# Performance work log

Measured on AMD Instinct MI355X. Metric: run time of the kernel, lower is better.

The kernel has to match this reference:

```python
import jax, jax.numpy as jnp
import numpy as np

D_MODEL = 768
N_CH = 2
D_STATE = 16
RANK = 8
LORA_SCALE = 2.0  # alpha/rank = (rank*2.0)/rank
N_LOOPS = 4       # MAX_INFER_LOOPS
BATCH = 1
SEQ = 1024
EPS = 1e-6        # RMSNorm eps


def setup_inputs() -> dict:
    key = jax.random.key(0)
    ks = jax.random.split(key, 12)
    f32 = jnp.float32
    n = lambda k, shp, s: jax.random.normal(k, shp, dtype=f32) * s
    return {
        "x": jax.random.normal(ks[0], (BATCH, SEQ, D_MODEL), dtype=f32),
        "in_proj_base": n(ks[1], (N_CH * D_MODEL, D_MODEL), 0.02),
        "lora_A": n(ks[2], (RANK, D_MODEL), 0.05),
        "lora_B": n(ks[3], (N_CH * D_MODEL, RANK), 0.05),
        "A_theta": n(ks[4], (N_CH, D_MODEL, D_STATE), 0.1),
        "B_real": n(ks[5], (N_CH, D_MODEL, D_STATE), 0.1),
        "B_imag": n(ks[6], (N_CH, D_MODEL, D_STATE), 0.1),
        "C_real": n(ks[7], (N_CH, D_MODEL, D_STATE), 0.1),
        "C_imag": n(ks[8], (N_CH, D_MODEL, D_STATE), 0.1),
        "out_proj_w": n(ks[9], (D_MODEL, N_CH * D_MODEL), 0.02),
        "mixer_norm_w": jnp.ones((D_MODEL,), f32),
        "loop_norm_w": jnp.ones((D_MODEL,), f32),
        "step_emb": n(ks[10], (N_LOOPS, D_MODEL), 0.02),
    }


def _rmsnorm(v, w):
    return v * jax.lax.rsqrt(jnp.mean(v * v, axis=-1, keepdims=True) + EPS) * w


def reference(x, in_proj_base, lora_A, lora_B, A_theta, B_real, B_imag,
              C_real, C_imag, out_proj_w, mixer_norm_w, loop_norm_w, step_emb):
    Bsz, Lsz, d = x.shape
    # LoRA-merged in_proj weight: base + scale * (B @ A)  [loop-invariant]
    W_in = in_proj_base + LORA_SCALE * (lora_B @ lora_A)  # [2d, d]
    cos_t = jnp.cos(A_theta)[None, None]  # [1,1,ch,d,s]
    sin_t = jnp.sin(A_theta)[None, None]
    Br = B_real[None, None]; Bi = B_imag[None, None]
    Cr = C_real[None, None]; Ci = C_imag[None, None]
    real = jnp.zeros((Bsz, Lsz, N_CH, d, D_STATE), x.dtype)
    imag = jnp.zeros_like(real)
    for i in range(N_LOOPS):  # fixed outer reasoning loop
        h = x + step_emb[i]
        # Mamba3ReasoningBlock: in_proj -> complex rotation state update -> sum over d_state
        x_in = (h @ W_in.T).reshape(Bsz, Lsz, N_CH, d)[..., None]  # [B,L,ch,d,1]
        new_real = cos_t * real - sin_t * imag + Br * x_in
        new_imag = sin_t * real + cos_t * imag + Bi * x_in
        y = (Cr * new_real - Ci * new_imag).sum(-1).reshape(Bsz, Lsz, N_CH * d)
        out = _rmsnorm(y @ out_proj_w.T, mixer_norm_w)
        x = _rmsnorm(h + out, loop_norm_w)  # residual + loop_norm
        real, imag = new_real, new_imag
    return x
```

## Files before the change

### kernel.cpp

```cpp
#include <hip/hip_runtime.h>

#define D_MODEL   768
#define TWO_D     1536
#define SEQ       1024
#define N_LOOPS   4
#define RANK      8
#define D_STATE   16
#define EPS       1e-6f

typedef unsigned short u16;
typedef short s16x8 __attribute__((ext_vector_type(8)));
typedef unsigned short u16x4 __attribute__((ext_vector_type(4)));
typedef float f32x4 __attribute__((ext_vector_type(4)));

__device__ inline u16 f2bf(float f) {
    union { float f; unsigned u; } v; v.f = f;
    unsigned r = v.u + 0x7fffu + ((v.u >> 16) & 1u);
    return (u16)(r >> 16);
}
__device__ inline float bf2f(u16 b) {
    union { unsigned u; float f; } v; v.u = ((unsigned)b) << 16;
    return v.f;
}

__global__ __launch_bounds__(256) void prep_all(
    const float* __restrict__ base, const float* __restrict__ lA,
    const float* __restrict__ lB,   const float* __restrict__ wout,
    const float* __restrict__ x,    const float* __restrict__ emb0,
    const float* __restrict__ th,   const float* __restrict__ Br,
    const float* __restrict__ Bi,   const float* __restrict__ Cr,
    const float* __restrict__ Ci,
    u16* __restrict__ Wbf, u16* __restrict__ Woutbf, float* __restrict__ G,
    float* __restrict__ hf, u16* __restrict__ hb)
{
    const int b = blockIdx.x, t = threadIdx.x;
    if (b < 1152) {
        int i0 = (b * 256 + t) * 4;
        int r = i0 / D_MODEL, c = i0 % D_MODEL;
        float4 a = *reinterpret_cast<const float4*>(&base[i0]);
#pragma unroll
        for (int k = 0; k < RANK; ++k) {
            float bk = 2.0f * lB[r * RANK + k];
            const float4 av = *reinterpret_cast<const float4*>(&lA[k * D_MODEL + c]);
            a.x += bk * av.x; a.y += bk * av.y; a.z += bk * av.z; a.w += bk * av.w;
        }
        u16x4 o; o.x = f2bf(a.x); o.y = f2bf(a.y); o.z = f2bf(a.z); o.w = f2bf(a.w);
        *reinterpret_cast<u16x4*>(&Wbf[i0]) = o;
    } else if (b < 2304) {
        int i0 = ((b - 1152) * 256 + t) * 4;
        const float4 v = *reinterpret_cast<const float4*>(&wout[i0]);
        u16x4 o; o.x = f2bf(v.x); o.y = f2bf(v.y); o.z = f2bf(v.z); o.w = f2bf(v.w);
        *reinterpret_cast<u16x4*>(&Woutbf[i0]) = o;
    } else if (b < 3072) {
        int i0 = ((b - 2304) * 256 + t) * 4;
        int d = i0 % D_MODEL;
        const float4 v = *reinterpret_cast<const float4*>(&x[i0]);
        const float4 e = *reinterpret_cast<const float4*>(&emb0[d]);
        float4 h = make_float4(v.x + e.x, v.y + e.y, v.z + e.z, v.w + e.w);
        *reinterpret_cast<float4*>(&hf[i0]) = h;
        u16x4 o; o.x = f2bf(h.x); o.y = f2bf(h.y); o.z = f2bf(h.z); o.w = f2bf(h.w);
        *reinterpret_cast<u16x4*>(&hb[i0]) = o;
    } else {
        int cd = (b - 3072) * 256 + t;
        if (cd >= TWO_D) return;
        float g0 = 0.f, g1 = 0.f, g2 = 0.f, g3 = 0.f;
        for (int s = 0; s < D_STATE; ++s) {
            int idx = cd * D_STATE + s;
            float tt = th[idx];
            float br = Br[idx], bi = Bi[idx];
            float cr = Cr[idx], ci = Ci[idx];
#pragma unroll
            for (int k = 0; k < 4; ++k) {
                float ck = cosf(k * tt), sk = sinf(k * tt);
                float er = ck * br - sk * bi;
                float ei = sk * br + ck * bi;
                float g  = cr * er - ci * ei;
                if (k == 0) g0 += g; else if (k == 1) g1 += g;
                else if (k == 2) g2 += g; else g3 += g;
            }
        }
        G[0 * TWO_D + cd] = g0; G[1 * TWO_D + cd] = g1;
        G[2 * TWO_D + cd] = g2; G[3 * TWO_D + cd] = g3;
    }
}

template<int K, int SPLITK, bool OUT_BF16>
__global__ __launch_bounds__(256) void gemm_nt(
    const u16* __restrict__ A, const u16* __restrict__ B,
    void* __restrict__ Cv, const int N)
{
    __shared__ u16 Al[64][72];
    __shared__ u16 Bl[64][72];
    const int t  = threadIdx.x;
    const int bm = blockIdx.y, bn = blockIdx.x, kz = blockIdx.z;
    const int lane = t & 63, w = t >> 6;
    const int wr = w >> 1, wc = w & 1;
    const int lr = lane & 15, kg = lane >> 4;

    const int KS = K / SPLITK;
    const int kbase = kz * KS;

    const int r0 = t >> 3;
    const int q0 = t & 7;
    const u16* Ag0 = A + (size_t)(bm * 64 + r0)      * K + kbase + q0 * 8;
    const u16* Ag1 = A + (size_t)(bm * 64 + r0 + 32) * K + kbase + q0 * 8;
    const u16* Bg0 = B + (size_t)(bn * 64 + r0)      * K + kbase + q0 * 8;
    const u16* Bg1 = B + (size_t)(bn * 64 + r0 + 32) * K + kbase + q0 * 8;

    uint4 ra0 = *reinterpret_cast<const uint4*>(Ag0);
    uint4 ra1 = *reinterpret_cast<const uint4*>(Ag1);
    uint4 rb0 = *reinterpret_cast<const uint4*>(Bg0);
    uint4 rb1 = *reinterpret_cast<const uint4*>(Bg1);

    f32x4 acc[2][2] = {};
    const int NKT = KS / 64;
    for (int kt = 0; kt < NKT; ++kt) {
        *reinterpret_cast<uint4*>(&Al[r0][q0 * 8])      = ra0;
        *reinterpret_cast<uint4*>(&Al[r0 + 32][q0 * 8]) = ra1;
        *reinterpret_cast<uint4*>(&Bl[r0][q0 * 8])      = rb0;
        *reinterpret_cast<uint4*>(&Bl[r0 + 32][q0 * 8]) = rb1;
        __syncthreads();
        if (kt + 1 < NKT) {
            const int ko = (kt + 1) * 64;
            ra0 = *reinterpret_cast<const uint4*>(Ag0 + ko);
            ra1 = *reinterpret_cast<const uint4*>(Ag1 + ko);
            rb0 = *reinterpret_cast<const uint4*>(Bg0 + ko);
            rb1 = *reinterpret_cast<const uint4*>(Bg1 + ko);
        }
#pragma unroll
        for (int ks = 0; ks < 2; ++ks) {
            const int ko = ks * 32 + kg * 8;
            s16x8 a0 = *reinterpret_cast<const s16x8*>(&Al[wr * 32 + lr][ko]);
            s16x8 a1 = *reinterpret_cast<const s16x8*>(&Al[wr * 32 + 16 + lr][ko]);
            s16x8 b0 = *reinterpret_cast<const s16x8*>(&Bl[wc * 32 + lr][ko]);
            s16x8 b1 = *reinterpret_cast<const s16x8*>(&Bl[wc * 32 + 16 + lr][ko]);
            acc[0][0] = __builtin_amdgcn_mfma_f32_16x16x32_bf16(a0, b0, acc[0][0], 0, 0, 0);
            acc[0][1] = __builtin_amdgcn_mfma_f32_16x16x32_bf16(a0, b1, acc[0][1], 0, 0, 0);
            acc[1][0] = __builtin_amdgcn_mfma_f32_16x16x32_bf16(a1, b0, acc[1][0], 0, 0, 0);
            acc[1][1] = __builtin_amdgcn_mfma_f32_16x16x32_bf16(a1, b1, acc[1][1], 0, 0, 0);
        }
        __syncthreads();
    }
    const int crow0 = bm * 64 + wr * 32 + kg * 4;
    const int ccol0 = bn * 64 + wc * 32 + lr;
#pragma unroll
    for (int m = 0; m < 2; ++m)
#pragma unroll
        for (int n = 0; n < 2; ++n)
#pragma unroll
            for (int r = 0; r < 4; ++r) {
                const int row = crow0 + m * 16 + r;
                const int col = ccol0 + n * 16;
                const float v = acc[m][n][r];
                if (OUT_BF16) ((u16*)Cv)[(size_t)row * N + col] = f2bf(v);
                else ((float*)Cv)[(size_t)kz * SEQ * N + (size_t)row * N + col] = v;
            }
}

__global__ __launch_bounds__(256) void y_kernel(
    const u16* __restrict__ xin,
    const float* __restrict__ G,
    const int nacc, u16* __restrict__ y)
{
    int i4 = blockIdx.x * 256 + threadIdx.x;
    int base = i4 * 4;
    int cd = base % TWO_D;
    float s0 = 0.f, s1 = 0.f, s2 = 0.f, s3 = 0.f;
    for (int j = 0; j < nacc; ++j) {
        u16x4 v = *reinterpret_cast<const u16x4*>(&xin[(size_t)j * SEQ * TWO_D + base]);
        const float4 g = *reinterpret_cast<const float4*>(&G[(size_t)(nacc - 1 - j) * TWO_D + cd]);
        s0 += bf2f(v.x) * g.x; s1 += bf2f(v.y) * g.y;
        s2 += bf2f(v.z) * g.z; s3 += bf2f(v.w) * g.w;
    }
    u16x4 o; o.x = f2bf(s0); o.y = f2bf(s1); o.z = f2bf(s2); o.w = f2bf(s3);
    *reinterpret_cast<u16x4*>(&y[base]) = o;
}

__global__ __launch_bounds__(256) void norm_kernel(
    const float* __restrict__ op0, const float* __restrict__ op1,
    const float* __restrict__ hprev,
    const float* __restrict__ mw,  const float* __restrict__ lw,
    const float* __restrict__ embn,
    float* __restrict__ dstf, u16* __restrict__ dstb)
{
    const int r = blockIdx.x * 4 + (threadIdx.x >> 6);
    const int lane = threadIdx.x & 63;
    const size_t ro = (size_t)r * D_MODEL;
    float op[12], h[12];
    float ss = 0.f;
#pragma unroll
    for (int e = 0; e < 12; ++e) {
        int d = lane + e * 64;
        op[e] = op0[ro + d] + op1[ro + d];
        h[e]  = hprev[ro + d];
        ss += op[e] * op[e];
    }
#pragma unroll
    for (int off = 32; off > 0; off >>= 1) ss += __shfl_xor(ss, off, 64);
    const float rs1 = rsqrtf(ss * (1.0f / D_MODEL) + EPS);
    float tt[12];
    float ss2 = 0.f;
#pragma unroll
    for (int e = 0; e < 12; ++e) {
        int d = lane + e * 64;
        tt[e] = h[e] + op[e] * rs1 * mw[d];
        ss2 += tt[e] * tt[e];
    }
#pragma unroll
    for (int off = 32; off > 0; off >>= 1) ss2 += __shfl_xor(ss2, off, 64);
    const float rs2 = rsqrtf(ss2 * (1.0f / D_MODEL) + EPS);
#pragma unroll
    for (int e = 0; e < 12; ++e) {
        int d = lane + e * 64;
        float xo = tt[e] * rs2 * lw[d];
        if (embn != nullptr) {
            float hn = xo + embn[d];
            dstf[ro + d] = hn;
            dstb[ro + d] = f2bf(hn);
        } else {
            dstf[ro + d] = xo;
        }
    }
}

extern "C" void kernel_launch(void* const* d_in, const int* in_sizes, int n_in,
                              void* d_out, int out_size, void* d_ws, size_t ws_size,
                              hipStream_t stream) {
    const float* x            = (const float*)d_in[0];
    const float* in_proj_base = (const float*)d_in[1];
    const float* lora_A       = (const float*)d_in[2];
    const float* lora_B       = (const float*)d_in[3];
    const float* A_theta      = (const float*)d_in[4];
    const float* B_real       = (const float*)d_in[5];
    const float* B_imag       = (const float*)d_in[6];
    const float* C_real       = (const float*)d_in[7];
    const float* C_imag       = (const float*)d_in[8];
    const float* out_proj_w   = (const float*)d_in[9];
    const float* mixer_w      = (const float*)d_in[10];
    const float* loop_w       = (const float*)d_in[11];
    const float* step_emb     = (const float*)d_in[12];
    float* out = (float*)d_out;

    char* p = (char*)d_ws;
    u16*   Wbf    = (u16*)p;   p += (size_t)TWO_D * D_MODEL * 2;
    u16*   Woutbf = (u16*)p;   p += (size_t)D_MODEL * TWO_D * 2;
    float* G      = (float*)p; p += (size_t)4 * TWO_D * 4;
    u16*   xin    = (u16*)p;   p += (size_t)N_LOOPS * SEQ * TWO_D * 2;
    u16*   ybf    = (u16*)p;   p += (size_t)SEQ * TWO_D * 2;
    float* hAf    = (float*)p; p += (size_t)SEQ * D_MODEL * 4;
    float* hBf    = (float*)p; p += (size_t)SEQ * D_MODEL * 4;
    u16*   hbf    = (u16*)p;   p += (size_t)SEQ * D_MODEL * 2;
    float* outpre = (float*)p; p += (size_t)2 * SEQ * D_MODEL * 4;

    prep_all<<<3078, 256, 0, stream>>>(
        in_proj_base, lora_A, lora_B, out_proj_w, x, step_emb,
        A_theta, B_real, B_imag, C_real, C_imag,
        Wbf, Woutbf, G, hAf, hbf);

    float* hcur = hAf;
    float* hnxt = hBf;
    for (int i = 0; i < N_LOOPS; ++i) {
        const bool last = (i == N_LOOPS - 1);
        gemm_nt<D_MODEL, 1, true><<<dim3(TWO_D / 64, SEQ / 64), 256, 0, stream>>>(
            hbf, Wbf, (void*)(xin + (size_t)i * SEQ * TWO_D), TWO_D);
        y_kernel<<<(SEQ * TWO_D / 4) / 256, 256, 0, stream>>>(xin, G, i + 1, ybf);
        gemm_nt<TWO_D, 2, false><<<dim3(D_MODEL / 64, SEQ / 64, 2), 256, 0, stream>>>(
            ybf, Woutbf, (void*)outpre, D_MODEL);
        norm_kernel<<<SEQ / 4, 256, 0, stream>>>(
            outpre, outpre + (size_t)SEQ * D_MODEL, hcur, mixer_w, loop_w,
            last ? nullptr : (step_emb + (size_t)(i + 1) * D_MODEL),
            last ? out : hnxt,
            last ? nullptr : hbf);
        float* tmp = hcur; hcur = hnxt; hnxt = tmp;
    }
}
```

Before: 228.7 us.

## Fold SSM coefficients into stacked out-proj weights and retile GEMM with direct LDS loads

Precomputes G-scaled copies of the out-projection weight for every loop lag and stores all in_proj outputs side by side. The out-projection GEMM then contracts over the concatenated history, so the separate y_kernel pass and its ybf buffer go away. The GEMM is retiled to 128x64 blocks and loads global data straight into LDS via global_load_lds, dropping the register-staged prefetch. The trade-off is a larger out-projection contraction that grows with the loop index, an unpadded LDS layout that may cause bank conflicts, and no overlap of loads with compute.

```diff
diff --git a/kernel.cpp b/kernel.cpp
--- a/kernel.cpp
+++ b/kernel.cpp
@@ -7,12 +7,22 @@
 #define RANK      8
 #define D_STATE   16
 #define EPS       1e-6f
+#define XIN_LD    (N_LOOPS * TWO_D)
 
 typedef unsigned short u16;
 typedef short s16x8 __attribute__((ext_vector_type(8)));
 typedef unsigned short u16x4 __attribute__((ext_vector_type(4)));
 typedef float f32x4 __attribute__((ext_vector_type(4)));
 
+#if defined(__has_builtin)
+#  if __has_builtin(__builtin_amdgcn_global_load_lds)
+#    define HAS_GLL 1
+#  endif
+#endif
+#ifndef HAS_GLL
+#  define HAS_GLL 0
+#endif
+
 __device__ inline u16 f2bf(float f) {
     union { float f; unsigned u; } v; v.f = f;
     unsigned r = v.u + 0x7fffu + ((v.u >> 16) & 1u);
@@ -23,14 +33,50 @@
     return v.f;
 }
 
+__device__ inline void gll16(const u16* g, u16* l) {
+#if HAS_GLL
+    __builtin_amdgcn_global_load_lds(
+        (__attribute__((address_space(1))) void*)(g),
+        (__attribute__((address_space(3))) void*)(l), 16, 0, 0);
+#else
+    const int ln = threadIdx.x & 63;
+    *reinterpret_cast<uint4*>(l + ln * 8) = *reinterpret_cast<const uint4*>(g);
+#endif
+}
+
+__global__ __launch_bounds__(256) void prep_g(
+    const float* __restrict__ th, const float* __restrict__ Br,
+    const float* __restrict__ Bi, const float* __restrict__ Cr,
+    const float* __restrict__ Ci, float* __restrict__ G)
+{
+    int cd = blockIdx.x * 256 + threadIdx.x;
+    if (cd >= TWO_D) return;
+    float g0 = 0.f, g1 = 0.f, g2 = 0.f, g3 = 0.f;
+    for (int s = 0; s < D_STATE; ++s) {
+        int idx = cd * D_STATE + s;
+        float tt = th[idx];
+        float br = Br[idx], bi = Bi[idx];
+        float cr = Cr[idx], ci = Ci[idx];
+#pragma unroll
+        for (int k = 0; k < 4; ++k) {
+            float ck = cosf(k * tt), sk = sinf(k * tt);
+            float er = ck * br - sk * bi;
+            float ei = sk * br + ck * bi;
+            float g  = cr * er - ci * ei;
+            if (k == 0) g0 += g; else if (k == 1) g1 += g;
+            else if (k == 2) g2 += g; else g3 += g;
+        }
+    }
+    G[0 * TWO_D + cd] = g0; G[1 * TWO_D + cd] = g1;
+    G[2 * TWO_D + cd] = g2; G[3 * TWO_D + cd] = g3;
+}
+
 __global__ __launch_bounds__(256) void prep_all(
     const float* __restrict__ base, const float* __restrict__ lA,
     const float* __restrict__ lB,   const float* __restrict__ wout,
     const float* __restrict__ x,    const float* __restrict__ emb0,
-    const float* __restrict__ th,   const float* __restrict__ Br,
-    const float* __restrict__ Bi,   const float* __restrict__ Cr,
-    const float* __restrict__ Ci,
-    u16* __restrict__ Wbf, u16* __restrict__ Woutbf, float* __restrict__ G,
+    const float* __restrict__ G,
+    u16* __restrict__ Wbf, u16* __restrict__ Wst,
     float* __restrict__ hf, u16* __restrict__ hb)
 {
     const int b = blockIdx.x, t = threadIdx.x;
@@ -46,13 +92,20 @@
         }
         u16x4 o; o.x = f2bf(a.x); o.y = f2bf(a.y); o.z = f2bf(a.z); o.w = f2bf(a.w);
         *reinterpret_cast<u16x4*>(&Wbf[i0]) = o;
-    } else if (b < 2304) {
+    } else if (b < 5760) {
         int i0 = ((b - 1152) * 256 + t) * 4;
-        const float4 v = *reinterpret_cast<const float4*>(&wout[i0]);
-        u16x4 o; o.x = f2bf(v.x); o.y = f2bf(v.y); o.z = f2bf(v.z); o.w = f2bf(v.w);
-        *reinterpret_cast<u16x4*>(&Woutbf[i0]) = o;
-    } else if (b < 3072) {
-        int i0 = ((b - 2304) * 256 + t) * 4;
+        int n = i0 / (4 * TWO_D);
+        int rem = i0 - n * 4 * TWO_D;
+        int m = rem / TWO_D;
+        int c = rem - m * TWO_D;
+        const float4 w = *reinterpret_cast<const float4*>(&wout[(size_t)n * TWO_D + c]);
+        const float4 g = *reinterpret_cast<const float4*>(&G[(size_t)(3 - m) * TWO_D + c]);
+        u16x4 o;
+        o.x = f2bf(w.x * g.x); o.y = f2bf(w.y * g.y);
+        o.z = f2bf(w.z * g.z); o.w = f2bf(w.w * g.w);
+        *reinterpret_cast<u16x4*>(&Wst[i0]) = o;
+    } else {
+        int i0 = ((b - 5760) * 256 + t) * 4;
         int d = i0 % D_MODEL;
         const float4 v = *reinterpret_cast<const float4*>(&x[i0]);
         const float4 e = *reinterpret_cast<const float4*>(&emb0[d]);
@@ -60,120 +113,68 @@
         *reinterpret_cast<float4*>(&hf[i0]) = h;
         u16x4 o; o.x = f2bf(h.x); o.y = f2bf(h.y); o.z = f2bf(h.z); o.w = f2bf(h.w);
         *reinterpret_cast<u16x4*>(&hb[i0]) = o;
-    } else {
-        int cd = (b - 3072) * 256 + t;
-        if (cd >= TWO_D) return;
-        float g0 = 0.f, g1 = 0.f, g2 = 0.f, g3 = 0.f;
-        for (int s = 0; s < D_STATE; ++s) {
-            int idx = cd * D_STATE + s;
-            float tt = th[idx];
-            float br = Br[idx], bi = Bi[idx];
-            float cr = Cr[idx], ci = Ci[idx];
-#pragma unroll
-            for (int k = 0; k < 4; ++k) {
-                float ck = cosf(k * tt), sk = sinf(k * tt);
-                float er = ck * br - sk * bi;
-                float ei = sk * br + ck * bi;
-                float g  = cr * er - ci * ei;
-                if (k == 0) g0 += g; else if (k == 1) g1 += g;
-                else if (k == 2) g2 += g; else g3 += g;
-            }
-        }
-        G[0 * TWO_D + cd] = g0; G[1 * TWO_D + cd] = g1;
-        G[2 * TWO_D + cd] = g2; G[3 * TWO_D + cd] = g3;
-    }
-}
-
-template<int K, int SPLITK, bool OUT_BF16>
+    }
+}
+
+template<bool OUT_BF16>
 __global__ __launch_bounds__(256) void gemm_nt(
-    const u16* __restrict__ A, const u16* __restrict__ B,
-    void* __restrict__ Cv, const int N)
-{
-    __shared__ u16 Al[64][72];
-    __shared__ u16 Bl[64][72];
-    const int t  = threadIdx.x;
+    const u16* __restrict__ A, const int lda,
+    const u16* __restrict__ B, const int ldb,
+    const int Kz, void* __restrict__ Cv, const int ldc)
+{
+    __shared__ __align__(16) u16 Al[128 * 64];
+    __shared__ __align__(16) u16 Bl[64 * 64];
+    const int t = threadIdx.x;
     const int bm = blockIdx.y, bn = blockIdx.x, kz = blockIdx.z;
     const int lane = t & 63, w = t >> 6;
-    const int wr = w >> 1, wc = w & 1;
+    const int wm = w >> 1, wn = w & 1;
     const int lr = lane & 15, kg = lane >> 4;
-
-    const int KS = K / SPLITK;
-    const int kbase = kz * KS;
-
-    const int r0 = t >> 3;
-    const int q0 = t & 7;
-    const u16* Ag0 = A + (size_t)(bm * 64 + r0)      * K + kbase + q0 * 8;
-    const u16* Ag1 = A + (size_t)(bm * 64 + r0 + 32) * K + kbase + q0 * 8;
-    const u16* Bg0 = B + (size_t)(bn * 64 + r0)      * K + kbase + q0 * 8;
-    const u16* Bg1 = B + (size_t)(bn * 64 + r0 + 32) * K + kbase + q0 * 8;
-
-    uint4 ra0 = *reinterpret_cast<const uint4*>(Ag0);
-    uint4 ra1 = *reinterpret_cast<const uint4*>(Ag1);
-    uint4 rb0 = *reinterpret_cast<const uint4*>(Bg0);
-    uint4 rb1 = *reinterpret_cast<const uint4*>(Bg1);
-
-    f32x4 acc[2][2] = {};
-    const int NKT = KS / 64;
-    for (int kt = 0; kt < NKT; ++kt) {
-        *reinterpret_cast<uint4*>(&Al[r0][q0 * 8])      = ra0;
-        *reinterpret_cast<uint4*>(&Al[r0 + 32][q0 * 8]) = ra1;
-        *reinterpret_cast<uint4*>(&Bl[r0][q0 * 8])      = rb0;
-        *reinterpret_cast<uint4*>(&Bl[r0 + 32][q0 * 8]) = rb1;
+    const int kbase = kz * Kz;
+
+    const u16* Aga = A + (size_t)(bm * 128 + w * 32 + (lane >> 3)) * lda + kbase + (lane & 7) * 8;
+    const u16* Bga = B + (size_t)(bn * 64  + w * 16 + (lane >> 3)) * ldb + kbase + (lane & 7) * 8;
+    u16* Alp = &Al[(w * 32) * 64];
+    u16* Blp = &Bl[(w * 16) * 64];
+
+    f32x4 acc[4][2] = {};
+    for (int k0 = 0; k0 < Kz; k0 += 64) {
+#pragma unroll
+        for (int q = 0; q < 4; ++q) gll16(Aga + (size_t)q * 8 * lda + k0, Alp + q * 512);
+#pragma unroll
+        for (int q = 0; q < 2; ++q) gll16(Bga + (size_t)q * 8 * ldb + k0, Blp + q * 512);
         __syncthreads();
-        if (kt + 1 < NKT) {
-            const int ko = (kt + 1) * 64;
-            ra0 = *reinterpret_cast<const uint4*>(Ag0 + ko);
-            ra1 = *reinterpret_cast<const uint4*>(Ag1 + ko);
-            rb0 = *reinterpret_cast<const uint4*>(Bg0 + ko);
-            rb1 = *reinterpret_cast<const uint4*>(Bg1 + ko);
-        }
 #pragma unroll
         for (int ks = 0; ks < 2; ++ks) {
-            const int ko = ks * 32 + kg * 8;
-            s16x8 a0 = *reinterpret_cast<const s16x8*>(&Al[wr * 32 + lr][ko]);
-            s16x8 a1 = *reinterpret_cast<const s16x8*>(&Al[wr * 32 + 16 + lr][ko]);
-            s16x8 b0 = *reinterpret_cast<const s16x8*>(&Bl[wc * 32 + lr][ko]);
-            s16x8 b1 = *reinterpret_cast<const s16x8*>(&Bl[wc * 32 + 16 + lr][ko]);
-            acc[0][0] = __builtin_amdgcn_mfma_f32_16x16x32_bf16(a0, b0, acc[0][0], 0, 0, 0);
-            acc[0][1] = __builtin_amdgcn_mfma_f32_16x16x32_bf16(a0, b1, acc[0][1], 0, 0, 0);
-            acc[1][0] = __builtin_amdgcn_mfma_f32_16x16x32_bf16(a1, b0, acc[1][0], 0, 0, 0);
-            acc[1][1] = __builtin_amdgcn_mfma_f32_16x16x32_bf16(a1, b1, acc[1][1], 0, 0, 0);
+            const int co = ks * 32 + kg * 8;
+            s16x8 a[4], b[2];
+#pragma unroll
+            for (int m = 0; m < 4; ++m)
+                a[m] = *reinterpret_cast<const s16x8*>(&Al[(wm * 64 + m * 16 + lr) * 64 + co]);
+#pragma unroll
+            for (int n = 0; n < 2; ++n)
+                b[n] = *reinterpret_cast<const s16x8*>(&Bl[(wn * 32 + n * 16 + lr) * 64 + co]);
+#pragma unroll
+            for (int m = 0; m < 4; ++m)
+#pragma unroll
+                for (int n = 0; n < 2; ++n)
+                    acc[m][n] = __builtin_amdgcn_mfma_f32_16x16x32_bf16(a[m], b[n], acc[m][n], 0, 0, 0);
         }
         __syncthreads();
     }
-    const int crow0 = bm * 64 + wr * 32 + kg * 4;
-    const int ccol0 = bn * 64 + wc * 32 + lr;
-#pragma unroll
-    for (int m = 0; m < 2; ++m)
+    const int row0 = bm * 128 + wm * 64 + kg * 4;
+    const int col0 = bn * 64 + wn * 32 + lr;
+#pragma unroll
+    for (int m = 0; m < 4; ++m)
 #pragma unroll
         for (int n = 0; n < 2; ++n)
 #pragma unroll
             for (int r = 0; r < 4; ++r) {
-                const int row = crow0 + m * 16 + r;
-                const int col = ccol0 + n * 16;
+                const int row = row0 + m * 16 + r;
+                const int col = col0 + n * 16;
                 const float v = acc[m][n][r];
-                if (OUT_BF16) ((u16*)Cv)[(size_t)row * N + col] = f2bf(v);
-                else ((float*)Cv)[(size_t)kz * SEQ * N + (size_t)row * N + col] = v;
+                if (OUT_BF16) ((u16*)Cv)[(size_t)row * ldc + col] = f2bf(v);
+                else ((float*)Cv)[(size_t)kz * SEQ * ldc + (size_t)row * ldc + col] = v;
             }
-}
-
-__global__ __launch_bounds__(256) void y_kernel(
-    const u16* __restrict__ xin,
-    const float* __restrict__ G,
-    const int nacc, u16* __restrict__ y)
-{
-    int i4 = blockIdx.x * 256 + threadIdx.x;
-    int base = i4 * 4;
-    int cd = base % TWO_D;
-    float s0 = 0.f, s1 = 0.f, s2 = 0.f, s3 = 0.f;
-    for (int j = 0; j < nacc; ++j) {
-        u16x4 v = *reinterpret_cast<const u16x4*>(&xin[(size_t)j * SEQ * TWO_D + base]);
-        const float4 g = *reinterpret_cast<const float4*>(&G[(size_t)(nacc - 1 - j) * TWO_D + cd]);
-        s0 += bf2f(v.x) * g.x; s1 += bf2f(v.y) * g.y;
-        s2 += bf2f(v.z) * g.z; s3 += bf2f(v.w) * g.w;
-    }
-    u16x4 o; o.x = f2bf(s0); o.y = f2bf(s1); o.z = f2bf(s2); o.w = f2bf(s3);
-    *reinterpret_cast<u16x4*>(&y[base]) = o;
 }
 
 __global__ __launch_bounds__(256) void norm_kernel(
@@ -243,34 +244,30 @@
 
     char* p = (char*)d_ws;
     u16*   Wbf    = (u16*)p;   p += (size_t)TWO_D * D_MODEL * 2;
-    u16*   Woutbf = (u16*)p;   p += (size_t)D_MODEL * TWO_D * 2;
+    u16*   Wst    = (u16*)p;   p += (size_t)D_MODEL * 4 * TWO_D * 2;
     float* G      = (float*)p; p += (size_t)4 * TWO_D * 4;
-    u16*   xin    = (u16*)p;   p += (size_t)N_LOOPS * SEQ * TWO_D * 2;
-    u16*   ybf    = (u16*)p;   p += (size_t)SEQ * TWO_D * 2;
-    float* hAf    = (float*)p; p += (size_t)SEQ * D_MODEL * 4;
-    float* hBf    = (float*)p; p += (size_t)SEQ * D_MODEL * 4;
+    u16*   xin    = (u16*)p;   p += (size_t)SEQ * XIN_LD * 2;
+    float* hf     = (float*)p; p += (size_t)SEQ * D_MODEL * 4;
     u16*   hbf    = (u16*)p;   p += (size_t)SEQ * D_MODEL * 2;
     float* outpre = (float*)p; p += (size_t)2 * SEQ * D_MODEL * 4;
 
-    prep_all<<<3078, 256, 0, stream>>>(
-        in_proj_base, lora_A, lora_B, out_proj_w, x, step_emb,
-        A_theta, B_real, B_imag, C_real, C_imag,
-        Wbf, Woutbf, G, hAf, hbf);
-
-    float* hcur = hAf;
-    float* hnxt = hBf;
+    prep_g<<<6, 256, 0, stream>>>(A_theta, B_real, B_imag, C_real, C_imag, G);
+    prep_all<<<6528, 256, 0, stream>>>(
+        in_proj_base, lora_A, lora_B, out_proj_w, x, step_emb, G,
+        Wbf, Wst, hf, hbf);
+
     for (int i = 0; i < N_LOOPS; ++i) {
         const bool last = (i == N_LOOPS - 1);
-        gemm_nt<D_MODEL, 1, true><<<dim3(TWO_D / 64, SEQ / 64), 256, 0, stream>>>(
-            hbf, Wbf, (void*)(xin + (size_t)i * SEQ * TWO_D), TWO_D);
-        y_kernel<<<(SEQ * TWO_D / 4) / 256, 256, 0, stream>>>(xin, G, i + 1, ybf);
-        gemm_nt<TWO_D, 2, false><<<dim3(D_MODEL / 64, SEQ / 64, 2), 256, 0, stream>>>(
-            ybf, Woutbf, (void*)outpre, D_MODEL);
+        gemm_nt<true><<<dim3(TWO_D / 64, SEQ / 128, 1), 256, 0, stream>>>(
+            hbf, D_MODEL, Wbf, D_MODEL, D_MODEL,
+            (void*)(xin + (size_t)i * TWO_D), XIN_LD);
+        gemm_nt<false><<<dim3(D_MODEL / 64, SEQ / 128, 2), 256, 0, stream>>>(
+            xin, XIN_LD, Wst + (size_t)(3 - i) * TWO_D, XIN_LD,
+            (i + 1) * D_MODEL, (void*)outpre, D_MODEL);
         norm_kernel<<<SEQ / 4, 256, 0, stream>>>(
-            outpre, outpre + (size_t)SEQ * D_MODEL, hcur, mixer_w, loop_w,
+            outpre, outpre + (size_t)SEQ * D_MODEL, hf, mixer_w, loop_w,
             last ? nullptr : (step_emb + (size_t)(i + 1) * D_MODEL),
-            last ? out : hnxt,
+            last ? out : hf,
             last ? nullptr : hbf);
-        float* tmp = hcur; hcur = hnxt; hnxt = tmp;
-    }
-}
+    }
+}
```

Measured after the change: 319.4 us. +39.7%, slower.

## Use direct global-to-LDS loads, raise split-K, fuse partial reduction into y kernel

Applied to the files above, without the earlier changes.

The GEMM now loads tiles with global_load_lds straight into unpadded LDS instead of staging through registers, and drops the register prefetch. The in-proj GEMM becomes split-K by 2 writing fp32 partials that y_kernel sums, rounds to bf16 and stores into the xin history. The out-proj uses split-K by 4, and norm_kernel reduces four partials. This adds blocks to fill more CUs, at the cost of extra fp32 partial traffic, no load/compute overlap, and possible LDS bank conflicts from removing the padding. norm now writes h in place, which is safe since each row reads before it writes.

```diff
diff --git a/kernel.cpp b/kernel.cpp
--- a/kernel.cpp
+++ b/kernel.cpp
@@ -13,6 +13,15 @@
 typedef unsigned short u16x4 __attribute__((ext_vector_type(4)));
 typedef float f32x4 __attribute__((ext_vector_type(4)));
 
+#if defined(__has_builtin)
+#  if __has_builtin(__builtin_amdgcn_global_load_lds)
+#    define HAS_GLL 1
+#  endif
+#endif
+#ifndef HAS_GLL
+#  define HAS_GLL 0
+#endif
+
 __device__ inline u16 f2bf(float f) {
     union { float f; unsigned u; } v; v.f = f;
     unsigned r = v.u + 0x7fffu + ((v.u >> 16) & 1u);
@@ -21,6 +30,17 @@
 __device__ inline float bf2f(u16 b) {
     union { unsigned u; float f; } v; v.u = ((unsigned)b) << 16;
     return v.f;
+}
+
+__device__ inline void gll16(const u16* g, u16* l) {
+#if HAS_GLL
+    __builtin_amdgcn_global_load_lds(
+        (__attribute__((address_space(1))) void*)(g),
+        (__attribute__((address_space(3))) void*)(l), 16, 0, 0);
+#else
+    const int ln = threadIdx.x & 63;
+    *reinterpret_cast<uint4*>(l + ln * 8) = *reinterpret_cast<const uint4*>(g);
+#endif
 }
 
 __global__ __launch_bounds__(256) void prep_all(
@@ -84,56 +104,39 @@
     }
 }
 
-template<int K, int SPLITK, bool OUT_BF16>
 __global__ __launch_bounds__(256) void gemm_nt(
-    const u16* __restrict__ A, const u16* __restrict__ B,
-    void* __restrict__ Cv, const int N)
-{
-    __shared__ u16 Al[64][72];
-    __shared__ u16 Bl[64][72];
-    const int t  = threadIdx.x;
+    const u16* __restrict__ A, const int lda,
+    const u16* __restrict__ B, const int ldb,
+    const int Kz, float* __restrict__ Cp, const int ldc)
+{
+    __shared__ __align__(16) u16 Al[64 * 64];
+    __shared__ __align__(16) u16 Bl[64 * 64];
+    const int t = threadIdx.x;
     const int bm = blockIdx.y, bn = blockIdx.x, kz = blockIdx.z;
     const int lane = t & 63, w = t >> 6;
     const int wr = w >> 1, wc = w & 1;
     const int lr = lane & 15, kg = lane >> 4;
-
-    const int KS = K / SPLITK;
-    const int kbase = kz * KS;
-
-    const int r0 = t >> 3;
-    const int q0 = t & 7;
-    const u16* Ag0 = A + (size_t)(bm * 64 + r0)      * K + kbase + q0 * 8;
-    const u16* Ag1 = A + (size_t)(bm * 64 + r0 + 32) * K + kbase + q0 * 8;
-    const u16* Bg0 = B + (size_t)(bn * 64 + r0)      * K + kbase + q0 * 8;
-    const u16* Bg1 = B + (size_t)(bn * 64 + r0 + 32) * K + kbase + q0 * 8;
-
-    uint4 ra0 = *reinterpret_cast<const uint4*>(Ag0);
-    uint4 ra1 = *reinterpret_cast<const uint4*>(Ag1);
-    uint4 rb0 = *reinterpret_cast<const uint4*>(Bg0);
-    uint4 rb1 = *reinterpret_cast<const uint4*>(Bg1);
+    const int kbase = kz * Kz;
+
+    const u16* Aga = A + (size_t)(bm * 64 + w * 16 + (lane >> 3)) * lda + kbase + (lane & 7) * 8;
+    const u16* Bga = B + (size_t)(bn * 64 + w * 16 + (lane >> 3)) * ldb + kbase + (lane & 7) * 8;
+    u16* Alp = &Al[(w * 16) * 64];
+    u16* Blp = &Bl[(w * 16) * 64];
 
     f32x4 acc[2][2] = {};
-    const int NKT = KS / 64;
-    for (int kt = 0; kt < NKT; ++kt) {
-        *reinterpret_cast<uint4*>(&Al[r0][q0 * 8])      = ra0;
-        *reinterpret_cast<uint4*>(&Al[r0 + 32][q0 * 8]) = ra1;
-        *reinterpret_cast<uint4*>(&Bl[r0][q0 * 8])      = rb0;
-        *reinterpret_cast<uint4*>(&Bl[r0 + 32][q0 * 8]) = rb1;
+    for (int k0 = 0; k0 < Kz; k0 += 64) {
+        gll16(Aga + k0, Alp);
+        gll16(Aga + (size_t)8 * lda + k0, Alp + 8 * 64);
+        gll16(Bga + k0, Blp);
+        gll16(Bga + (size_t)8 * ldb + k0, Blp + 8 * 64);
         __syncthreads();
-        if (kt + 1 < NKT) {
-            const int ko = (kt + 1) * 64;
-            ra0 = *reinterpret_cast<const uint4*>(Ag0 + ko);
-            ra1 = *reinterpret_cast<const uint4*>(Ag1 + ko);
-            rb0 = *reinterpret_cast<const uint4*>(Bg0 + ko);
-            rb1 = *reinterpret_cast<const uint4*>(Bg1 + ko);
-        }
 #pragma unroll
         for (int ks = 0; ks < 2; ++ks) {
-            const int ko = ks * 32 + kg * 8;
-            s16x8 a0 = *reinterpret_cast<const s16x8*>(&Al[wr * 32 + lr][ko]);
-            s16x8 a1 = *reinterpret_cast<const s16x8*>(&Al[wr * 32 + 16 + lr][ko]);
-            s16x8 b0 = *reinterpret_cast<const s16x8*>(&Bl[wc * 32 + lr][ko]);
-            s16x8 b1 = *reinterpret_cast<const s16x8*>(&Bl[wc * 32 + 16 + lr][ko]);
+            const int co = ks * 32 + kg * 8;
+            s16x8 a0 = *reinterpret_cast<const s16x8*>(&Al[(wr * 32 +      lr) * 64 + co]);
+            s16x8 a1 = *reinterpret_cast<const s16x8*>(&Al[(wr * 32 + 16 + lr) * 64 + co]);
+            s16x8 b0 = *reinterpret_cast<const s16x8*>(&Bl[(wc * 32 +      lr) * 64 + co]);
+            s16x8 b1 = *reinterpret_cast<const s16x8*>(&Bl[(wc * 32 + 16 + lr) * 64 + co]);
             acc[0][0] = __builtin_amdgcn_mfma_f32_16x16x32_bf16(a0, b0, acc[0][0], 0, 0, 0);
             acc[0][1] = __builtin_amdgcn_mfma_f32_16x16x32_bf16(a0, b1, acc[0][1], 0, 0, 0);
             acc[1][0] = __builtin_amdgcn_mfma_f32_16x16x32_bf16(a1, b0, acc[1][0], 0, 0, 0);
@@ -141,34 +144,37 @@
         }
         __syncthreads();
     }
-    const int crow0 = bm * 64 + wr * 32 + kg * 4;
-    const int ccol0 = bn * 64 + wc * 32 + lr;
+    const int row0 = bm * 64 + wr * 32 + kg * 4;
+    const int col0 = bn * 64 + wc * 32 + lr;
+    float* Cz = Cp + (size_t)kz * SEQ * ldc;
 #pragma unroll
     for (int m = 0; m < 2; ++m)
 #pragma unroll
         for (int n = 0; n < 2; ++n)
 #pragma unroll
-            for (int r = 0; r < 4; ++r) {
-                const int row = crow0 + m * 16 + r;
-                const int col = ccol0 + n * 16;
-                const float v = acc[m][n][r];
-                if (OUT_BF16) ((u16*)Cv)[(size_t)row * N + col] = f2bf(v);
-                else ((float*)Cv)[(size_t)kz * SEQ * N + (size_t)row * N + col] = v;
-            }
+            for (int r = 0; r < 4; ++r)
+                Cz[(size_t)(row0 + m * 16 + r) * ldc + col0 + n * 16] = acc[m][n][r];
 }
 
 __global__ __launch_bounds__(256) void y_kernel(
-    const u16* __restrict__ xin,
+    const float* __restrict__ p,
+    u16* __restrict__ xin,
     const float* __restrict__ G,
-    const int nacc, u16* __restrict__ y)
+    const int li, u16* __restrict__ y)
 {
     int i4 = blockIdx.x * 256 + threadIdx.x;
     int base = i4 * 4;
     int cd = base % TWO_D;
-    float s0 = 0.f, s1 = 0.f, s2 = 0.f, s3 = 0.f;
-    for (int j = 0; j < nacc; ++j) {
+    const float4 v0 = *reinterpret_cast<const float4*>(&p[base]);
+    const float4 v1 = *reinterpret_cast<const float4*>(&p[(size_t)SEQ * TWO_D + base]);
+    float4 s = make_float4(v0.x + v1.x, v0.y + v1.y, v0.z + v1.z, v0.w + v1.w);
+    u16x4 xo; xo.x = f2bf(s.x); xo.y = f2bf(s.y); xo.z = f2bf(s.z); xo.w = f2bf(s.w);
+    *reinterpret_cast<u16x4*>(&xin[(size_t)li * SEQ * TWO_D + base]) = xo;
+    const float4 g0 = *reinterpret_cast<const float4*>(&G[cd]);
+    float s0 = g0.x * s.x, s1 = g0.y * s.y, s2 = g0.z * s.z, s3 = g0.w * s.w;
+    for (int j = 0; j < li; ++j) {
         u16x4 v = *reinterpret_cast<const u16x4*>(&xin[(size_t)j * SEQ * TWO_D + base]);
-        const float4 g = *reinterpret_cast<const float4*>(&G[(size_t)(nacc - 1 - j) * TWO_D + cd]);
+        const float4 g = *reinterpret_cast<const float4*>(&G[(size_t)(li - j) * TWO_D + cd]);
         s0 += bf2f(v.x) * g.x; s1 += bf2f(v.y) * g.y;
         s2 += bf2f(v.z) * g.z; s3 += bf2f(v.w) * g.w;
     }
@@ -177,7 +183,7 @@
 }
 
 __global__ __launch_bounds__(256) void norm_kernel(
-    const float* __restrict__ op0, const float* __restrict__ op1,
+    const float* __restrict__ q,
     const float* __restrict__ hprev,
     const float* __restrict__ mw,  const float* __restrict__ lw,
     const float* __restrict__ embn,
@@ -186,12 +192,13 @@
     const int r = blockIdx.x * 4 + (threadIdx.x >> 6);
     const int lane = threadIdx.x & 63;
     const size_t ro = (size_t)r * D_MODEL;
+    const size_t PS = (size_t)SEQ * D_MODEL;
     float op[12], h[12];
     float ss = 0.f;
 #pragma unroll
     for (int e = 0; e < 12; ++e) {
         int d = lane + e * 64;
-        op[e] = op0[ro + d] + op1[ro + d];
+        op[e] = (q[ro + d] + q[PS + ro + d]) + (q[2 * PS + ro + d] + q[3 * PS + ro + d]);
         h[e]  = hprev[ro + d];
         ss += op[e] * op[e];
     }
@@ -241,36 +248,33 @@
     const float* step_emb     = (const float*)d_in[12];
     float* out = (float*)d_out;
 
-    char* p = (char*)d_ws;
-    u16*   Wbf    = (u16*)p;   p += (size_t)TWO_D * D_MODEL * 2;
-    u16*   Woutbf = (u16*)p;   p += (size_t)D_MODEL * TWO_D * 2;
-    float* G      = (float*)p; p += (size_t)4 * TWO_D * 4;
-    u16*   xin    = (u16*)p;   p += (size_t)N_LOOPS * SEQ * TWO_D * 2;
-    u16*   ybf    = (u16*)p;   p += (size_t)SEQ * TWO_D * 2;
-    float* hAf    = (float*)p; p += (size_t)SEQ * D_MODEL * 4;
-    float* hBf    = (float*)p; p += (size_t)SEQ * D_MODEL * 4;
-    u16*   hbf    = (u16*)p;   p += (size_t)SEQ * D_MODEL * 2;
-    float* outpre = (float*)p; p += (size_t)2 * SEQ * D_MODEL * 4;
+    char* p8 = (char*)d_ws;
+    u16*   Wbf    = (u16*)p8;   p8 += (size_t)TWO_D * D_MODEL * 2;
+    u16*   Woutbf = (u16*)p8;   p8 += (size_t)D_MODEL * TWO_D * 2;
+    float* G      = (float*)p8; p8 += (size_t)4 * TWO_D * 4;
+    u16*   xin    = (u16*)p8;   p8 += (size_t)N_LOOPS * SEQ * TWO_D * 2;
+    u16*   ybf    = (u16*)p8;   p8 += (size_t)SEQ * TWO_D * 2;
+    float* hf     = (float*)p8; p8 += (size_t)SEQ * D_MODEL * 4;
+    u16*   hbf    = (u16*)p8;   p8 += (size_t)SEQ * D_MODEL * 2;
+    float* pbuf   = (float*)p8; p8 += (size_t)2 * SEQ * TWO_D * 4;
+    float* qbuf   = (float*)p8; p8 += (size_t)4 * SEQ * D_MODEL * 4;
 
     prep_all<<<3078, 256, 0, stream>>>(
         in_proj_base, lora_A, lora_B, out_proj_w, x, step_emb,
         A_theta, B_real, B_imag, C_real, C_imag,
-        Wbf, Woutbf, G, hAf, hbf);
-
-    float* hcur = hAf;
-    float* hnxt = hBf;
+        Wbf, Woutbf, G, hf, hbf);
+
     for (int i = 0; i < N_LOOPS; ++i) {
         const bool last = (i == N_LOOPS - 1);
-        gemm_nt<D_MODEL, 1, true><<<dim3(TWO_D / 64, SEQ / 64), 256, 0, stream>>>(
-            hbf, Wbf, (void*)(xin + (size_t)i * SEQ * TWO_D), TWO_D);
-        y_kernel<<<(SEQ * TWO_D / 4) / 256, 256, 0, stream>>>(xin, G, i + 1, ybf);
-        gemm_nt<TWO_D, 2, false><<<dim3(D_MODEL / 64, SEQ / 64, 2), 256, 0, stream>>>(
-            ybf, Woutbf, (void*)outpre, D_MODEL);
+        gemm_nt<<<dim3(TWO_D / 64, SEQ / 64, 2), 256, 0, stream>>>(
+            hbf, D_MODEL, Wbf, D_MODEL, D_MODEL / 2, pbuf, TWO_D);
+        y_kernel<<<(SEQ * TWO_D / 4) / 256, 256, 0, stream>>>(pbuf, xin, G, i, ybf);
+        gemm_nt<<<dim3(D_MODEL / 64, SEQ / 64, 4), 256, 0, stream>>>(
+            ybf, TWO_D, Woutbf, TWO_D, TWO_D / 4, qbuf, D_MODEL);
         norm_kernel<<<SEQ / 4, 256, 0, stream>>>(
-            outpre, outpre + (size_t)SEQ * D_MODEL, hcur, mixer_w, loop_w,
+            qbuf, hf, mixer_w, loop_w,
             last ? nullptr : (step_emb + (size_t)(i + 1) * D_MODEL),
-            last ? out : hnxt,
+            last ? out : hf,
             last ? nullptr : hbf);
-        float* tmp = hcur; hcur = hnxt; hnxt = tmp;
-    }
-}
+    }
+}
```

New measurement: 234.1 us. 2.4% more time.
